# Performance work log

Hardware: AMD Instinct MI355X
Metric: run time of the kernel (lower is better)

Reference implementation:

```python
import jax, jax.numpy as jnp
import numpy as np

N_NODES = 100000
N_EDGES = 1600000
D_IN = 128
D_OUT = 128
EPS = 1e-5


def setup_inputs() -> dict:
    key = jax.random.key(0)
    ks = jax.random.split(key, 5)
    x = jax.random.normal(ks[0], (N_NODES, D_IN), dtype=jnp.float32)
    edge_index = jax.random.randint(ks[1], (2, N_EDGES), 0, N_NODES, dtype=jnp.int64)
    scale = 1.0 / np.sqrt(D_IN)
    W_root = jax.random.normal(ks[2], (D_IN, D_OUT), dtype=jnp.float32) * scale
    W_rel = jax.random.normal(ks[3], (D_IN, D_OUT), dtype=jnp.float32) * scale
    b_rel = jax.random.normal(ks[4], (D_OUT,), dtype=jnp.float32) * 0.01
    gamma = jnp.ones((D_OUT,), dtype=jnp.float32)
    beta = jnp.zeros((D_OUT,), dtype=jnp.float32)
    return {"x": x, "edge_index": edge_index, "W_root": W_root, "W_rel": W_rel,
            "b_rel": b_rel, "gamma": gamma, "beta": beta}


def reference(x, edge_index, W_root, W_rel, b_rel, gamma, beta):
    # GraphConv: out = aggr(x_j) @ W_rel + b_rel + x @ W_root   (aggr = sum)
    src = edge_index[0]
    dst = edge_index[1]
    aggr = jax.ops.segment_sum(x[src], dst, num_segments=x.shape[0])  # [N, D_IN]
    h = aggr @ W_rel + b_rel + x @ W_root                              # [N, D_OUT]
    # NodeLevelBatchNorm (training mode: batch stats over node dim, biased var)
    mean = jnp.mean(h, axis=0)
    var = jnp.mean(jnp.square(h - mean), axis=0)
    h_norm = (h - mean) * jax.lax.rsqrt(var + EPS) * gamma + beta
    return jax.nn.relu(h_norm)
```

## Files before the change

### kernel.cpp

```cpp
#include <hip/hip_runtime.h>

#define N_NODES 100000
#define N_EDGES 1600000
#define D 128
#define NB 196
#define EPT 10
#define CHUNK 2560
#define BIN_BLOCKS 625
#define CVT_X_BLOCKS 6250

typedef __bf16 bf16x8 __attribute__((ext_vector_type(8)));
typedef float f32x4 __attribute__((ext_vector_type(4)));

__device__ __forceinline__ unsigned f2bf(float f) {
    unsigned u = __float_as_uint(f);
    return (u + 0x7fffu + ((u >> 16) & 1u)) >> 16;
}
__device__ __forceinline__ float bf_lo(unsigned u) { return __uint_as_float(u << 16); }
__device__ __forceinline__ float bf_hi(unsigned u) { return __uint_as_float(u & 0xffff0000u); }

__global__ __launch_bounds__(256) void prep_kernel(const float* __restrict__ x,
                                                   const float* __restrict__ Wrel,
                                                   const float* __restrict__ Wroot,
                                                   const int* __restrict__ ei,
                                                   unsigned short* __restrict__ x_bf,
                                                   unsigned short* __restrict__ Wt,
                                                   int* __restrict__ bcount) {
    __shared__ int h[256];
    int b = blockIdx.x;
    int t = threadIdx.x;
    if (b < CVT_X_BLOCKS) {
        size_t i = ((size_t)b * 256 + t) * 8;
        float4 v0 = *(const float4*)(x + i);
        float4 v1 = *(const float4*)(x + i + 4);
        uint4 p;
        p.x = f2bf(v0.x) | (f2bf(v0.y) << 16);
        p.y = f2bf(v0.z) | (f2bf(v0.w) << 16);
        p.z = f2bf(v1.x) | (f2bf(v1.y) << 16);
        p.w = f2bf(v1.z) | (f2bf(v1.w) << 16);
        *(uint4*)(x_bf + i) = p;
    } else if (b < CVT_X_BLOCKS + 128) {
        int c = b - CVT_X_BLOCKS;
        float v = (t < 128) ? Wrel[t * D + c] : Wroot[(t - 128) * D + c];
        Wt[c * 256 + t] = (unsigned short)f2bf(v);
    } else {
        int blk = b - (CVT_X_BLOCKS + 128);
        h[t] = 0;
        __syncthreads();
        int base = blk * CHUNK;
#pragma unroll
        for (int i = 0; i < EPT; ++i) {
            int dst = ei[N_EDGES + base + i * 256 + t];
            atomicAdd(&h[dst >> 9], 1);
        }
        __syncthreads();
        if (t < NB && h[t]) atomicAdd(&bcount[t], h[t]);
    }
}

__global__ __launch_bounds__(256) void bscan_kernel(const int* __restrict__ bcount,
                                                    int* __restrict__ bucket_base,
                                                    int* __restrict__ bcur) {
    __shared__ int s[256];
    int t = threadIdx.x;
    int v = (t < NB) ? bcount[t] : 0;
    s[t] = v;
    __syncthreads();
    for (int off = 1; off < 256; off <<= 1) {
        int a = (t >= off) ? s[t - off] : 0;
        __syncthreads();
        s[t] += a;
        __syncthreads();
    }
    int excl = s[t] - v;
    if (t < NB) {
        bucket_base[t] = excl;
        bcur[t] = excl;
    }
    if (t == NB) bucket_base[NB] = N_EDGES;
}

__global__ __launch_bounds__(256) void binify_kernel(const int* __restrict__ ei,
                                                     int* __restrict__ bcur,
                                                     unsigned* __restrict__ epk) {
    __shared__ int lhist[256];
    __shared__ int lstart[256];
    __shared__ int lfill[256];
    __shared__ int gbase[256];
    __shared__ uint2 stage[CHUNK];

    int t = threadIdx.x;
    int base = blockIdx.x * CHUNK;
    lhist[t] = 0;
    lfill[t] = 0;
    __syncthreads();

    int src[EPT], dst[EPT];
#pragma unroll
    for (int i = 0; i < EPT; ++i) {
        int e = base + i * 256 + t;
        src[i] = ei[e];
        dst[i] = ei[N_EDGES + e];
        atomicAdd(&lhist[dst[i] >> 9], 1);
    }
    __syncthreads();

    int v = lhist[t];
    lstart[t] = v;
    __syncthreads();
    for (int off = 1; off < 256; off <<= 1) {
        int a = (t >= off) ? lstart[t - off] : 0;
        __syncthreads();
        lstart[t] += a;
        __syncthreads();
    }
    int excl = lstart[t] - v;
    if (t < NB && v > 0) gbase[t] = atomicAdd(&bcur[t], v);
    __syncthreads();
    lstart[t] = excl;
    __syncthreads();

#pragma unroll
    for (int i = 0; i < EPT; ++i) {
        int b = dst[i] >> 9;
        int lp = atomicAdd(&lfill[b], 1);
        stage[lstart[b] + lp] = make_uint2((unsigned)src[i], (unsigned)dst[i]);
    }
    __syncthreads();

    for (int i = t; i < CHUNK; i += 256) {
        uint2 p = stage[i];
        int b = (int)(p.y >> 9);
        unsigned code = p.x | ((p.y & 511u) << 17);
        epk[gbase[b] + (i - lstart[b])] = code;
    }
}

__global__ __launch_bounds__(256) void place_kernel(const unsigned* __restrict__ epk,
                                                    const int* __restrict__ bucket_base,
                                                    int* __restrict__ rowstart,
                                                    int* __restrict__ srcs) {
    __shared__ int bufA[512];
    __shared__ int bufB[512];
    int b = blockIdx.x;
    int t = threadIdx.x;
    int pbeg = bucket_base[b];
    int pend = bucket_base[b + 1];

    bufA[t] = 0;
    bufA[t + 256] = 0;
    __syncthreads();
    for (int i = pbeg + t; i < pend; i += 256)
        atomicAdd(&bufA[epk[i] >> 17], 1);
    __syncthreads();

    for (int j = t; j < 512; j += 256) bufB[j] = j ? bufA[j - 1] : 0;
    __syncthreads();
    int* cur = bufB;
    int* nxt = bufA;
    for (int off = 1; off < 512; off <<= 1) {
        for (int j = t; j < 512; j += 256)
            nxt[j] = cur[j] + ((j >= off) ? cur[j - off] : 0);
        __syncthreads();
        int* tmp = cur; cur = nxt; nxt = tmp;
    }

    for (int j = t; j < 512; j += 256) {
        int gnode = (b << 9) + j;
        int val = pbeg + cur[j];
        if (gnode <= N_NODES) rowstart[gnode] = val;
        nxt[j] = val;
    }
    __syncthreads();

    for (int i = pbeg + t; i < pend; i += 256) {
        unsigned code = epk[i];
        int pos = atomicAdd(&nxt[code >> 17], 1);
        srcs[pos] = (int)(code & 0x1FFFFu);
    }
}

__global__ __launch_bounds__(256) void gather_kernel(const unsigned short* __restrict__ x_bf,
                                                     const int* __restrict__ rowstart,
                                                     const int* __restrict__ srcs,
                                                     unsigned short* __restrict__ aggr_bf) {
    int t = threadIdx.x;
    int node = blockIdx.x * 8 + (t >> 5);
    int lane = t & 31;
    int begin = rowstart[node];
    int end = rowstart[node + 1];
    const unsigned short* xp = x_bf + lane * 4;
    float a0 = 0.f, a1 = 0.f, a2 = 0.f, a3 = 0.f;
    int e = begin;
    for (; e + 7 < end; e += 8) {
        int s0 = srcs[e],     s1 = srcs[e + 1], s2 = srcs[e + 2], s3 = srcs[e + 3];
        int s4 = srcs[e + 4], s5 = srcs[e + 5], s6 = srcs[e + 6], s7 = srcs[e + 7];
        uint2 u0 = *(const uint2*)(xp + (size_t)s0 * D);
        uint2 u1 = *(const uint2*)(xp + (size_t)s1 * D);
        uint2 u2 = *(const uint2*)(xp + (size_t)s2 * D);
        uint2 u3 = *(const uint2*)(xp + (size_t)s3 * D);
        uint2 u4 = *(const uint2*)(xp + (size_t)s4 * D);
        uint2 u5 = *(const uint2*)(xp + (size_t)s5 * D);
        uint2 u6 = *(const uint2*)(xp + (size_t)s6 * D);
        uint2 u7 = *(const uint2*)(xp + (size_t)s7 * D);
        a0 += bf_lo(u0.x) + bf_lo(u1.x) + bf_lo(u2.x) + bf_lo(u3.x)
            + bf_lo(u4.x) + bf_lo(u5.x) + bf_lo(u6.x) + bf_lo(u7.x);
        a1 += bf_hi(u0.x) + bf_hi(u1.x) + bf_hi(u2.x) + bf_hi(u3.x)
            + bf_hi(u4.x) + bf_hi(u5.x) + bf_hi(u6.x) + bf_hi(u7.x);
        a2 += bf_lo(u0.y) + bf_lo(u1.y) + bf_lo(u2.y) + bf_lo(u3.y)
            + bf_lo(u4.y) + bf_lo(u5.y) + bf_lo(u6.y) + bf_lo(u7.y);
        a3 += bf_hi(u0.y) + bf_hi(u1.y) + bf_hi(u2.y) + bf_hi(u3.y)
            + bf_hi(u4.y) + bf_hi(u5.y) + bf_hi(u6.y) + bf_hi(u7.y);
    }
    for (; e + 1 < end; e += 2) {
        int s0 = srcs[e], s1 = srcs[e + 1];
        uint2 u0 = *(const uint2*)(xp + (size_t)s0 * D);
        uint2 u1 = *(const uint2*)(xp + (size_t)s1 * D);
        a0 += bf_lo(u0.x) + bf_lo(u1.x);
        a1 += bf_hi(u0.x) + bf_hi(u1.x);
        a2 += bf_lo(u0.y) + bf_lo(u1.y);
        a3 += bf_hi(u0.y) + bf_hi(u1.y);
    }
    if (e < end) {
        uint2 u = *(const uint2*)(xp + (size_t)srcs[e] * D);
        a0 += bf_lo(u.x);
        a1 += bf_hi(u.x);
        a2 += bf_lo(u.y);
        a3 += bf_hi(u.y);
    }
    uint2 w;
    w.x = f2bf(a0) | (f2bf(a1) << 16);
    w.y = f2bf(a2) | (f2bf(a3) << 16);
    *(uint2*)(aggr_bf + (size_t)node * D + lane * 4) = w;
}

#define LDSTRIDE 40
__global__ __launch_bounds__(256) void gemm_mfma(const unsigned short* __restrict__ aggr_bf,
                                                 const unsigned short* __restrict__ x_bf,
                                                 const unsigned short* __restrict__ Wt,
                                                 const float* __restrict__ brel,
                                                 unsigned short* __restrict__ h_bf,
                                                 float* __restrict__ gsum,
                                                 float* __restrict__ gss) {
    __shared__ unsigned short As[128][LDSTRIDE];
    __shared__ unsigned short Bs[128][LDSTRIDE];
    __shared__ float sbias[128];
    __shared__ float SredS[4][128];
    __shared__ float SredQ[4][128];

    const int t = threadIdx.x;
    const int wave = t >> 6;
    const int lane = t & 63;
    const int quad = lane >> 4;
    const int l16 = lane & 15;
    const int blockRow = blockIdx.x * 128;

    if (t < 128) sbias[t] = brel[t];

    f32x4 acc[2][8];
#pragma unroll
    for (int i = 0; i < 2; ++i)
#pragma unroll
        for (int j = 0; j < 8; ++j) acc[i][j] = (f32x4){0.f, 0.f, 0.f, 0.f};

    for (int kc = 0; kc < 8; ++kc) {
        const unsigned short* Asrc = (kc < 4) ? aggr_bf : x_bf;
        const int k0 = (kc & 3) * 32;
#pragma unroll
        for (int s = t; s < 512; s += 256) {
            int row = s >> 2;
            int q = (s & 3) * 8;
            int grow = blockRow + row;
            uint4 v = make_uint4(0, 0, 0, 0);
            if (grow < N_NODES) v = *(const uint4*)(Asrc + (size_t)grow * D + k0 + q);
            *(uint4*)&As[row][q] = v;
        }
#pragma unroll
        for (int s = t; s < 512; s += 256) {
            int col = s >> 2;
            int q = (s & 3) * 8;
            uint4 v = *(const uint4*)(Wt + col * 256 + kc * 32 + q);
            *(uint4*)&Bs[col][q] = v;
        }
        __syncthreads();

        bf16x8 afrag0 = *(bf16x8*)&As[wave * 32 + l16][quad * 8];
        bf16x8 afrag1 = *(bf16x8*)&As[wave * 32 + 16 + l16][quad * 8];
#pragma unroll
        for (int ct = 0; ct < 8; ++ct) {
            bf16x8 bfrag = *(bf16x8*)&Bs[ct * 16 + l16][quad * 8];
            acc[0][ct] = __builtin_amdgcn_mfma_f32_16x16x32_bf16(afrag0, bfrag, acc[0][ct], 0, 0, 0);
            acc[1][ct] = __builtin_amdgcn_mfma_f32_16x16x32_bf16(afrag1, bfrag, acc[1][ct], 0, 0, 0);
        }
        __syncthreads();
    }

    float csum[8], css[8];
#pragma unroll
    for (int ct = 0; ct < 8; ++ct) { csum[ct] = 0.f; css[ct] = 0.f; }

#pragma unroll
    for (int rt = 0; rt < 2; ++rt) {
#pragma unroll
        for (int ct = 0; ct < 8; ++ct) {
            int col = ct * 16 + l16;
            float bv = sbias[col];
#pragma unroll
            for (int reg = 0; reg < 4; ++reg) {
                int row = blockRow + wave * 32 + rt * 16 + quad * 4 + reg;
                if (row < N_NODES) {
                    float v = acc[rt][ct][reg] + bv;
                    h_bf[(size_t)row * D + col] = (unsigned short)f2bf(v);
                    csum[ct] += v;
                    css[ct] += v * v;
                }
            }
        }
    }
#pragma unroll
    for (int ct = 0; ct < 8; ++ct) {
        float s = csum[ct], q = css[ct];
        s += __shfl_xor(s, 16);
        s += __shfl_xor(s, 32);
        q += __shfl_xor(q, 16);
        q += __shfl_xor(q, 32);
        if (quad == 0) {
            SredS[wave][ct * 16 + l16] = s;
            SredQ[wave][ct * 16 + l16] = q;
        }
    }
    __syncthreads();
    if (t < 128) {
        float s = SredS[0][t] + SredS[1][t] + SredS[2][t] + SredS[3][t];
        float q = SredQ[0][t] + SredQ[1][t] + SredQ[2][t] + SredQ[3][t];
        unsafeAtomicAdd(&gsum[t], s);
        unsafeAtomicAdd(&gss[t], q);
    }
}

__global__ __launch_bounds__(256) void norm_kernel(const unsigned short* __restrict__ h_bf,
                                                   float* __restrict__ out,
                                                   const float* __restrict__ gsum,
                                                   const float* __restrict__ gss,
                                                   const float* __restrict__ gamma,
                                                   const float* __restrict__ beta) {
    __shared__ float sscale[128];
    __shared__ float sshift[128];
    int t = threadIdx.x;
    if (t < 128) {
        const float inv_n = 1.0f / (float)N_NODES;
        float mean = gsum[t] * inv_n;
        float var = gss[t] * inv_n - mean * mean;
        float rs = rsqrtf(var + 1e-5f);
        float sc = gamma[t] * rs;
        sscale[t] = sc;
        sshift[t] = beta[t] - mean * sc;
    }
    __syncthreads();
    size_t e = ((size_t)blockIdx.x * 256 + t) * 4;
    if (e >= (size_t)N_NODES * D) return;
    int c = (int)(e & 127);
    uint2 u = *(const uint2*)(h_bf + e);
    float4 v;
    v.x = fmaxf(bf_lo(u.x) * sscale[c + 0] + sshift[c + 0], 0.f);
    v.y = fmaxf(bf_hi(u.x) * sscale[c + 1] + sshift[c + 1], 0.f);
    v.z = fmaxf(bf_lo(u.y) * sscale[c + 2] + sshift[c + 2], 0.f);
    v.w = fmaxf(bf_hi(u.y) * sscale[c + 3] + sshift[c + 3], 0.f);
    *(float4*)(out + e) = v;
}

extern "C" void kernel_launch(void* const* d_in, const int* in_sizes, int n_in,
                              void* d_out, int out_size, void* d_ws, size_t ws_size,
                              hipStream_t stream) {
    const float* x     = (const float*)d_in[0];
    const int*   ei    = (const int*)d_in[1];
    const float* Wroot = (const float*)d_in[2];
    const float* Wrel  = (const float*)d_in[3];
    const float* brel  = (const float*)d_in[4];
    const float* gamma = (const float*)d_in[5];
    const float* beta  = (const float*)d_in[6];
    float* out = (float*)d_out;

    unsigned short* aggr_bf = (unsigned short*)d_ws;
    unsigned short* x_bf    = aggr_bf + (size_t)N_NODES * D;
    unsigned short* Wt      = x_bf + (size_t)N_NODES * D;
    float* gsum  = (float*)(Wt + 128 * 256);
    float* gss   = gsum + 128;
    int* bcount  = (int*)(gss + 128);
    int* bucket_base = bcount + 256;
    int* bcur    = bucket_base + 256;
    int* rowstart = bcur + 256;
    unsigned* epk = (unsigned*)(rowstart + 100352);
    int* srcs    = (int*)(epk + N_EDGES);
    unsigned short* h_bf = (unsigned short*)epk;

    hipMemsetAsync(gsum, 0, 512 * sizeof(int), stream);

    prep_kernel<<<CVT_X_BLOCKS + 128 + BIN_BLOCKS, 256, 0, stream>>>(
        x, Wrel, Wroot, ei, x_bf, Wt, bcount);
    bscan_kernel<<<1, 256, 0, stream>>>(bcount, bucket_base, bcur);
    binify_kernel<<<BIN_BLOCKS, 256, 0, stream>>>(ei, bcur, epk);
    place_kernel<<<NB, 256, 0, stream>>>(epk, bucket_base, rowstart, srcs);
    gather_kernel<<<N_NODES / 8, 256, 0, stream>>>(x_bf, rowstart, srcs, aggr_bf);
    gemm_mfma<<<(N_NODES + 127) / 128, 256, 0, stream>>>(aggr_bf, x_bf, Wt, brel, h_bf, gsum, gss);
    norm_kernel<<<12500, 256, 0, stream>>>(h_bf, out, gsum, gss, gamma, beta);
}
```

Before: 292.3 us.

## Restructure GEMM to 64-row tiles with K=64 chunks and register prefetch

The fused dual GEMM now uses 64-row blocks with K chunks of 64, so there are 4 iterations instead of 8. Each iteration prefetches the next A/B chunk into registers while the MFMAs on the current chunk run. The reduction scratch now reuses the A tile's shared memory. This aims to cut barrier count, hide global load latency and raise the number of blocks for better occupancy, at the cost of reloading W twice as often per output row.

```diff
diff --git a/kernel.cpp b/kernel.cpp
--- a/kernel.cpp
+++ b/kernel.cpp
@@ -234,7 +234,7 @@
     *(uint2*)(aggr_bf + (size_t)node * D + lane * 4) = w;
 }
 
-#define LDSTRIDE 40
+#define ASTRIDE 72
 __global__ __launch_bounds__(256) void gemm_mfma(const unsigned short* __restrict__ aggr_bf,
                                                  const unsigned short* __restrict__ x_bf,
                                                  const unsigned short* __restrict__ Wt,
@@ -242,55 +242,93 @@
                                                  unsigned short* __restrict__ h_bf,
                                                  float* __restrict__ gsum,
                                                  float* __restrict__ gss) {
-    __shared__ unsigned short As[128][LDSTRIDE];
-    __shared__ unsigned short Bs[128][LDSTRIDE];
+    __shared__ unsigned short As[64][ASTRIDE];
+    __shared__ unsigned short Bs[128][ASTRIDE];
     __shared__ float sbias[128];
-    __shared__ float SredS[4][128];
-    __shared__ float SredQ[4][128];
 
     const int t = threadIdx.x;
     const int wave = t >> 6;
     const int lane = t & 63;
     const int quad = lane >> 4;
     const int l16 = lane & 15;
-    const int blockRow = blockIdx.x * 128;
+    const int blockRow = blockIdx.x * 64;
 
     if (t < 128) sbias[t] = brel[t];
 
-    f32x4 acc[2][8];
-#pragma unroll
-    for (int i = 0; i < 2; ++i)
-#pragma unroll
-        for (int j = 0; j < 8; ++j) acc[i][j] = (f32x4){0.f, 0.f, 0.f, 0.f};
-
-    for (int kc = 0; kc < 8; ++kc) {
-        const unsigned short* Asrc = (kc < 4) ? aggr_bf : x_bf;
-        const int k0 = (kc & 3) * 32;
-#pragma unroll
-        for (int s = t; s < 512; s += 256) {
-            int row = s >> 2;
-            int q = (s & 3) * 8;
+    const int ar0 = t >> 3;
+    const int aq0 = (t & 7) * 8;
+    const int ar1 = (t + 256) >> 3;
+
+    uint4 pa[2], pb[4];
+
+    {
+        const unsigned short* Asrc = aggr_bf;
+#pragma unroll
+        for (int r = 0; r < 2; ++r) {
+            int row = (t + 256 * r) >> 3;
+            int q = (t & 7) * 8;
             int grow = blockRow + row;
-            uint4 v = make_uint4(0, 0, 0, 0);
-            if (grow < N_NODES) v = *(const uint4*)(Asrc + (size_t)grow * D + k0 + q);
-            *(uint4*)&As[row][q] = v;
-        }
-#pragma unroll
-        for (int s = t; s < 512; s += 256) {
-            int col = s >> 2;
-            int q = (s & 3) * 8;
-            uint4 v = *(const uint4*)(Wt + col * 256 + kc * 32 + q);
-            *(uint4*)&Bs[col][q] = v;
-        }
-        __syncthreads();
-
-        bf16x8 afrag0 = *(bf16x8*)&As[wave * 32 + l16][quad * 8];
-        bf16x8 afrag1 = *(bf16x8*)&As[wave * 32 + 16 + l16][quad * 8];
-#pragma unroll
-        for (int ct = 0; ct < 8; ++ct) {
-            bf16x8 bfrag = *(bf16x8*)&Bs[ct * 16 + l16][quad * 8];
-            acc[0][ct] = __builtin_amdgcn_mfma_f32_16x16x32_bf16(afrag0, bfrag, acc[0][ct], 0, 0, 0);
-            acc[1][ct] = __builtin_amdgcn_mfma_f32_16x16x32_bf16(afrag1, bfrag, acc[1][ct], 0, 0, 0);
+            pa[r] = make_uint4(0, 0, 0, 0);
+            if (grow < N_NODES) pa[r] = *(const uint4*)(Asrc + (size_t)grow * D + q);
+        }
+#pragma unroll
+        for (int r = 0; r < 4; ++r) {
+            int s = t + 256 * r;
+            int col = s >> 3;
+            int q = (s & 7) * 8;
+            pb[r] = *(const uint4*)(Wt + col * 256 + q);
+        }
+    }
+
+    f32x4 acc[8];
+#pragma unroll
+    for (int j = 0; j < 8; ++j) acc[j] = (f32x4){0.f, 0.f, 0.f, 0.f};
+
+    for (int it = 0; it < 4; ++it) {
+#pragma unroll
+        for (int r = 0; r < 2; ++r) {
+            int row = (t + 256 * r) >> 3;
+            int q = (t & 7) * 8;
+            *(uint4*)&As[row][q] = pa[r];
+        }
+#pragma unroll
+        for (int r = 0; r < 4; ++r) {
+            int s = t + 256 * r;
+            int col = s >> 3;
+            int q = (s & 7) * 8;
+            *(uint4*)&Bs[col][q] = pb[r];
+        }
+        __syncthreads();
+
+        if (it < 3) {
+            int nit = it + 1;
+            const unsigned short* Asrc = (nit < 2) ? aggr_bf : x_bf;
+            int kk = (nit & 1) * 64;
+#pragma unroll
+            for (int r = 0; r < 2; ++r) {
+                int row = (t + 256 * r) >> 3;
+                int q = (t & 7) * 8;
+                int grow = blockRow + row;
+                pa[r] = make_uint4(0, 0, 0, 0);
+                if (grow < N_NODES) pa[r] = *(const uint4*)(Asrc + (size_t)grow * D + kk + q);
+            }
+#pragma unroll
+            for (int r = 0; r < 4; ++r) {
+                int s = t + 256 * r;
+                int col = s >> 3;
+                int q = (s & 7) * 8;
+                pb[r] = *(const uint4*)(Wt + col * 256 + nit * 64 + q);
+            }
+        }
+
+#pragma unroll
+        for (int ks = 0; ks < 2; ++ks) {
+            bf16x8 afrag = *(bf16x8*)&As[wave * 16 + l16][ks * 32 + quad * 8];
+#pragma unroll
+            for (int ct = 0; ct < 8; ++ct) {
+                bf16x8 bfrag = *(bf16x8*)&Bs[ct * 16 + l16][ks * 32 + quad * 8];
+                acc[ct] = __builtin_amdgcn_mfma_f32_16x16x32_bf16(afrag, bfrag, acc[ct], 0, 0, 0);
+            }
         }
         __syncthreads();
     }
@@ -300,23 +338,24 @@
     for (int ct = 0; ct < 8; ++ct) { csum[ct] = 0.f; css[ct] = 0.f; }
 
 #pragma unroll
-    for (int rt = 0; rt < 2; ++rt) {
-#pragma unroll
-        for (int ct = 0; ct < 8; ++ct) {
-            int col = ct * 16 + l16;
-            float bv = sbias[col];
-#pragma unroll
-            for (int reg = 0; reg < 4; ++reg) {
-                int row = blockRow + wave * 32 + rt * 16 + quad * 4 + reg;
-                if (row < N_NODES) {
-                    float v = acc[rt][ct][reg] + bv;
-                    h_bf[(size_t)row * D + col] = (unsigned short)f2bf(v);
-                    csum[ct] += v;
-                    css[ct] += v * v;
-                }
+    for (int ct = 0; ct < 8; ++ct) {
+        int col = ct * 16 + l16;
+        float bv = sbias[col];
+#pragma unroll
+        for (int reg = 0; reg < 4; ++reg) {
+            int row = blockRow + wave * 16 + quad * 4 + reg;
+            if (row < N_NODES) {
+                float v = acc[ct][reg] + bv;
+                h_bf[(size_t)row * D + col] = (unsigned short)f2bf(v);
+                csum[ct] += v;
+                css[ct] += v * v;
             }
         }
     }
+
+    float* SredS = (float*)&As[0][0];
+    float* SredQ = SredS + 512;
+    __syncthreads();
 #pragma unroll
     for (int ct = 0; ct < 8; ++ct) {
         float s = csum[ct], q = css[ct];
@@ -325,14 +364,14 @@
         q += __shfl_xor(q, 16);
         q += __shfl_xor(q, 32);
         if (quad == 0) {
-            SredS[wave][ct * 16 + l16] = s;
-            SredQ[wave][ct * 16 + l16] = q;
+            SredS[wave * 128 + ct * 16 + l16] = s;
+            SredQ[wave * 128 + ct * 16 + l16] = q;
         }
     }
     __syncthreads();
     if (t < 128) {
-        float s = SredS[0][t] + SredS[1][t] + SredS[2][t] + SredS[3][t];
-        float q = SredQ[0][t] + SredQ[1][t] + SredQ[2][t] + SredQ[3][t];
+        float s = SredS[t] + SredS[128 + t] + SredS[256 + t] + SredS[384 + t];
+        float q = SredQ[t] + SredQ[128 + t] + SredQ[256 + t] + SredQ[384 + t];
         unsafeAtomicAdd(&gsum[t], s);
         unsafeAtomicAdd(&gss[t], q);
     }
@@ -402,6 +441,6 @@
     binify_kernel<<<BIN_BLOCKS, 256, 0, stream>>>(ei, bcur, epk);
     place_kernel<<<NB, 256, 0, stream>>>(epk, bucket_base, rowstart, srcs);
     gather_kernel<<<N_NODES / 8, 256, 0, stream>>>(x_bf, rowstart, srcs, aggr_bf);
-    gemm_mfma<<<(N_NODES + 127) / 128, 256, 0, stream>>>(aggr_bf, x_bf, Wt, brel, h_bf, gsum, gss);
+    gemm_mfma<<<(N_NODES + 63) / 64, 256, 0, stream>>>(aggr_bf, x_bf, Wt, brel, h_bf, gsum, gss);
     norm_kernel<<<12500, 256, 0, stream>>>(h_bf, out, gsum, gss, gamma, beta);
 }
```

After: 308.5 us. 1.06x slower.
